# Optimization experiments

Measured on AMD Instinct MI355X. Metric: run time of the kernel, lower is better.

The kernel has to match this reference:

```python
import jax, jax.numpy as jnp
import numpy as np

# Insertion order of keys == output channel order (matches OrderedDict in torch module)
MAPPING = {
    "nodata": [0],
    "water": [1, 2, 3],
    "forest": [4, 5, 6, 7, 8, 9, 10, 11, 12, 13],
    "shrub": [14, 15, 16, 17, 18, 19],
    "grass": [20, 21, 22, 23, 24, 25, 26, 27],
    "crop": [28, 29, 30, 31, 32, 33, 34, 35, 36, 37],
    "urban": [38, 39, 40, 41, 42, 43, 44, 45],
    "bare": [46, 47, 48, 49, 50, 51],
    "wetland": [52, 53, 54, 55, 56],
    "snow": [57, 58],
    "moss": [59, 60, 61],
    "cloud": [62, 63],
}
B, C, H, W = 8, 64, 512, 512
K = len(MAPPING)
# static gather indices: flat channel index and its group id
_IDX = np.concatenate([np.asarray(v, dtype=np.int32) for v in MAPPING.values()])
_GID = np.concatenate([np.full(len(v), g, dtype=np.int32) for g, v in enumerate(MAPPING.values())])


def setup_inputs() -> dict:
    key = jax.random.key(0)
    pred_lr = jax.random.normal(key, (B, C, H, W), dtype=jnp.float32)
    # conv heads are mean-initialized: weight = 1/len(group), bias = 0
    weights = jnp.concatenate([
        jnp.full((len(v),), 1.0 / max(1, len(v)), dtype=jnp.float32)
        for v in MAPPING.values()
    ])  # [sum(len(group))] == [64]
    biases = jnp.zeros((K,), dtype=jnp.float32)
    return {"pred_lr": pred_lr, "weights": weights, "biases": biases}


def reference(pred_lr, weights, biases):
    # Equivalent to: for each group g, 1x1 conv over gathered channels pred_lr[:, idxs]
    # Expressed as one sparse (scattered) K x C mixing matrix -> single contraction.
    Wmat = jnp.zeros((K, C), dtype=weights.dtype).at[_GID, _IDX].set(weights)
    pred_hr = jnp.einsum('bchw,kc->bkhw', pred_lr, Wmat) + biases[None, :, None, None]
    return pred_hr  # [B, K, H, W]; class names = list(MAPPING.keys())
```

## Files before the change

kernel.cpp:

```cpp
#include <hip/hip_runtime.h>


#define NB 8
#define NC 64
#define NK 12
#define NP (512 * 512)
#define NPV (NP / 4)
#define F4_PER_THREAD 2
#define BLOCK 256
#define TILE (BLOCK * F4_PER_THREAD)
#define BLOCKS_PER_B (NPV / TILE)

typedef float v4f __attribute__((ext_vector_type(4)));

__global__ __launch_bounds__(BLOCK) void
hier_invert_kernel(const float* __restrict__ in,
                   const float* __restrict__ w,
                   const float* __restrict__ bias,
                   float* __restrict__ out) {
    const int tid = threadIdx.x;
    const int b    = blockIdx.x >> 7;
    const int pblk = (blockIdx.x & 127) << 9;
    const int p = pblk + tid;

    const v4f* __restrict__ in4 =
        (const v4f*)in + (long long)b * NC * NPV + p;
    v4f* __restrict__ out4 =
        (v4f*)out + (long long)b * NK * NPV + p;

    constexpr int gs[NK + 1] = {0, 1, 4, 14, 20, 28, 38, 46, 52, 57, 59, 62, 64};

#pragma unroll
    for (int k = 0; k < NK; ++k) {
        const float bk = bias[k];
        v4f acc0 = {bk, bk, bk, bk};
        v4f acc1 = acc0;
#pragma unroll
        for (int c = gs[k]; c < gs[k + 1]; ++c) {
            const float wc = w[c];
            const v4f v0 = __builtin_nontemporal_load(&in4[(long long)c * NPV]);
            const v4f v1 = __builtin_nontemporal_load(&in4[(long long)c * NPV + BLOCK]);
            acc0 += wc * v0;
            acc1 += wc * v1;
        }
        __builtin_nontemporal_store(acc0, &out4[(long long)k * NPV]);
        __builtin_nontemporal_store(acc1, &out4[(long long)k * NPV + BLOCK]);
    }
}

extern "C" void kernel_launch(void* const* d_in, const int* in_sizes, int n_in,
                              void* d_out, int out_size, void* d_ws, size_t ws_size,
                              hipStream_t stream) {
    const float* in   = (const float*)d_in[0];
    const float* w    = (const float*)d_in[1];
    const float* bias = (const float*)d_in[2];
    float* out        = (float*)d_out;

    const int grid = NB * BLOCKS_PER_B;
    hier_invert_kernel<<<grid, BLOCK, 0, stream>>>(in, w, bias, out);
}
```

Before: 686.8 us.

## Split work per output group across blocks and batch group loads upfront

Measured after the change: 680.1 us. No clear change (-1.0%).

```diff
diff --git a/kernel.cpp b/kernel.cpp
--- a/kernel.cpp
+++ b/kernel.cpp
@@ -4,14 +4,35 @@
 #define NB 8
 #define NC 64
 #define NK 12
-#define NP (512 * 512)
-#define NPV (NP / 4)
+#define NPV 65536
+#define BLOCK 256
 #define F4_PER_THREAD 2
-#define BLOCK 256
 #define TILE (BLOCK * F4_PER_THREAD)
-#define BLOCKS_PER_B (NPV / TILE)
+#define TPP (NPV / TILE)
 
 typedef float v4f __attribute__((ext_vector_type(4)));
+
+template <int C0, int CNT>
+__device__ __forceinline__ void
+group_body(const v4f* __restrict__ in4, v4f* __restrict__ out4,
+           const float* __restrict__ w, float bk) {
+    v4f v0[CNT], v1[CNT];
+#pragma unroll
+    for (int i = 0; i < CNT; ++i) {
+        v0[i] = __builtin_nontemporal_load(&in4[(long long)(C0 + i) * NPV]);
+        v1[i] = __builtin_nontemporal_load(&in4[(long long)(C0 + i) * NPV + BLOCK]);
+    }
+    v4f acc0 = {bk, bk, bk, bk};
+    v4f acc1 = acc0;
+#pragma unroll
+    for (int i = 0; i < CNT; ++i) {
+        const float wc = w[C0 + i];
+        acc0 += wc * v0[i];
+        acc1 += wc * v1[i];
+    }
+    __builtin_nontemporal_store(acc0, &out4[0]);
+    __builtin_nontemporal_store(acc1, &out4[BLOCK]);
+}
 
 __global__ __launch_bounds__(BLOCK) void
 hier_invert_kernel(const float* __restrict__ in,
@@ -19,32 +40,33 @@
                    const float* __restrict__ bias,
                    float* __restrict__ out) {
     const int tid = threadIdx.x;
-    const int b    = blockIdx.x >> 7;
-    const int pblk = (blockIdx.x & 127) << 9;
-    const int p = pblk + tid;
+    int id = blockIdx.x;
+    const int t = id & (TPP - 1);
+    id >>= 7;
+    const int k = id % NK;
+    const int b = id / NK;
+    const int p = (t << 9) + tid;
 
     const v4f* __restrict__ in4 =
         (const v4f*)in + (long long)b * NC * NPV + p;
     v4f* __restrict__ out4 =
-        (v4f*)out + (long long)b * NK * NPV + p;
+        (v4f*)out + (long long)(b * NK + k) * NPV + p;
 
-    constexpr int gs[NK + 1] = {0, 1, 4, 14, 20, 28, 38, 46, 52, 57, 59, 62, 64};
+    const float bk = bias[k];
 
-#pragma unroll
-    for (int k = 0; k < NK; ++k) {
-        const float bk = bias[k];
-        v4f acc0 = {bk, bk, bk, bk};
-        v4f acc1 = acc0;
-#pragma unroll
-        for (int c = gs[k]; c < gs[k + 1]; ++c) {
-            const float wc = w[c];
-            const v4f v0 = __builtin_nontemporal_load(&in4[(long long)c * NPV]);
-            const v4f v1 = __builtin_nontemporal_load(&in4[(long long)c * NPV + BLOCK]);
-            acc0 += wc * v0;
-            acc1 += wc * v1;
-        }
-        __builtin_nontemporal_store(acc0, &out4[(long long)k * NPV]);
-        __builtin_nontemporal_store(acc1, &out4[(long long)k * NPV + BLOCK]);
+    switch (k) {
+        case 0:  group_body<0, 1>(in4, out4, w, bk);  break;
+        case 1:  group_body<1, 3>(in4, out4, w, bk);  break;
+        case 2:  group_body<4, 10>(in4, out4, w, bk); break;
+        case 3:  group_body<14, 6>(in4, out4, w, bk); break;
+        case 4:  group_body<20, 8>(in4, out4, w, bk); break;
+        case 5:  group_body<28, 10>(in4, out4, w, bk); break;
+        case 6:  group_body<38, 8>(in4, out4, w, bk); break;
+        case 7:  group_body<46, 6>(in4, out4, w, bk); break;
+        case 8:  group_body<52, 5>(in4, out4, w, bk); break;
+        case 9:  group_body<57, 2>(in4, out4, w, bk); break;
+        case 10: group_body<59, 3>(in4, out4, w, bk); break;
+        default: group_body<62, 2>(in4, out4, w, bk); break;
     }
 }
 
@@ -56,6 +78,6 @@
     const float* bias = (const float*)d_in[2];
     float* out        = (float*)d_out;
 
-    const int grid = NB * BLOCKS_PER_B;
+    const int grid = NB * NK * TPP;
     hier_invert_kernel<<<grid, BLOCK, 0, stream>>>(in, w, bias, out);
 }
```
